# Optimization experiments

Measured on AMD Instinct MI355X. Metric: run time of the kernel, lower is better.

## Reference

```python
import jax, jax.numpy as jnp
import numpy as np

N = 10000      # nodes
E = 160000     # edges
F = 128        # feature multiplicity (num_features)
NSPEC = 10     # species
NL = 2         # interaction layers
R_MAX = 5.0
NB = 8         # bessel basis size
HR = 64        # radial MLP hidden
EPS = 0.5      # epsilon scaling
SH_DIM = 16    # l=0..3 -> 1+3+5+7
L_OF_LM = np.array([0, 1, 1, 1, 2, 2, 2, 2, 2, 3, 3, 3, 3, 3, 3, 3])
SLICES = [(0, 1), (1, 4), (4, 9), (9, 16)]  # (start,end) per l block


def _sh16(u):
    """Real spherical harmonics l=0..3, component normalization (sum_m Y^2 = 2l+1). u: [E,3] unit vectors."""
    x, y, z = u[:, 0], u[:, 1], u[:, 2]
    one = jnp.ones_like(x)
    s3, s5, s7, s15, s42, s70, s105 = map(lambda v: float(np.sqrt(v)), (3, 5, 7, 15, 42, 70, 105))
    ys = [
        one,
        s3 * x, s3 * y, s3 * z,
        s15 * x * y, s15 * y * z, 0.5 * s5 * (3 * z * z - 1.0), s15 * x * z, 0.5 * s15 * (x * x - y * y),
        0.25 * s70 * y * (3 * x * x - y * y),
        s105 * x * y * z,
        0.25 * s42 * y * (5 * z * z - 1.0),
        0.5 * s7 * (5 * z ** 3 - 3 * z),
        0.25 * s42 * x * (5 * z * z - 1.0),
        0.5 * s105 * z * (x * x - y * y),
        0.25 * s70 * x * (x * x - 3 * y * y),
    ]
    return jnp.stack(ys, axis=-1)  # [E,16]


def _radial(r):
    """Bessel radial basis with smooth cosine cutoff. r: [E,1] -> [E,NB]."""
    n = jnp.arange(1, NB + 1, dtype=r.dtype)
    f = jnp.sqrt(2.0 / R_MAX) * jnp.sin(n * jnp.pi * r / R_MAX) / jnp.maximum(r, 1e-9)
    cut = 0.5 * (jnp.cos(jnp.pi * jnp.clip(r, 0.0, R_MAX) / R_MAX) + 1.0)
    return f * cut


def setup_inputs() -> dict:
    key = jax.random.key(0)
    ks = jax.random.split(key, 16)
    d = {}
    d["vectors"] = jax.random.normal(ks[0], (E, 3), jnp.float32) * 1.5
    d["node_specie"] = jax.random.randint(ks[1], (N,), 0, NSPEC, jnp.int32)
    d["senders"] = jax.random.randint(ks[2], (E,), 0, N, jnp.int32)
    d["receivers"] = jax.random.randint(ks[3], (E,), 0, N, jnp.int32)
    d["emb_W"] = jax.random.normal(ks[4], (NSPEC, F), jnp.float32)
    d["radial_W1"] = jax.random.normal(ks[5], (NL, NB, HR), jnp.float32) / np.sqrt(NB)
    d["radial_b1"] = jnp.zeros((NL, HR), jnp.float32)
    d["radial_W2"] = jax.random.normal(ks[6], (NL, HR, F * 4), jnp.float32) / np.sqrt(HR)
    d["lin_W"] = jax.random.normal(ks[7], (NL, NSPEC, 4, F, F), jnp.float32) / np.sqrt(F)
    d["prod_c"] = jax.random.normal(ks[8], (NL, NSPEC, 3, F), jnp.float32) * 0.3
    d["sc_W"] = jax.random.normal(ks[9], (NL, NSPEC, 4, F, F), jnp.float32) / np.sqrt(F)
    d["ro0_W"] = jax.random.normal(ks[10], (F, 1), jnp.float32) / np.sqrt(F)
    d["ro1_W1"] = jax.random.normal(ks[11], (F, 16), jnp.float32) / np.sqrt(F)
    d["ro1_W2"] = jax.random.normal(ks[12], (16, 1), jnp.float32) / 4.0
    return d


def _species_linear(feats, W):
    # feats: [N,F,16], W: [N,4,F,F] (per-l linear). out[n,g,lm] = sum_f feats[n,f,lm] W[n,l(lm),f,g]
    outs = [jnp.einsum("nfm,nfg->ngm", feats[:, :, a:b], W[:, l]) for l, (a, b) in enumerate(SLICES)]
    return jnp.concatenate(outs, axis=-1)


def reference(vectors, node_specie, senders, receivers, emb_W, radial_W1, radial_b1,
              radial_W2, lin_W, prod_c, sc_W, ro0_W, ro1_W1, ro1_W2):
    lengths = jnp.maximum(jnp.linalg.norm(vectors, axis=-1, keepdims=True), 1e-9)  # [E,1]
    sh = _sh16(vectors / lengths)          # [E,16] edge attrs
    edge_feats = _radial(lengths)          # [E,NB]

    # node embedding: scalars only (l=0 slot)
    feats = jnp.zeros((N, F, SH_DIM), vectors.dtype).at[:, :, 0].set(emb_W[node_specie])
    lmap = jnp.asarray(L_OF_LM)
    outputs = []
    for i in range(NL):
        # radial MLP -> per-(feature,l) tensor-product weights
        h = jax.nn.silu(edge_feats @ radial_W1[i] + radial_b1[i])
        rw = (h @ radial_W2[i]).reshape(E, F, 4)          # [E,F,4]
        sender_scalars = feats[senders, :, 0]             # gather, [E,F]
        # per-edge tensor product: scalar x SH weighted by radial weights
        msg = sender_scalars[:, :, None] * rw[:, :, lmap] * sh[:, None, :]   # [E,F,16]
        agg = jax.ops.segment_sum(msg, receivers, num_segments=N)           # scatter-sum, [N,F,16]
        new = _species_linear(agg, lin_W[i][node_specie]) * EPS
        # residual self-connection (per-species linear) for layers > 0
        sc = None if i == 0 else _species_linear(feats, sc_W[i][node_specie])
        # product basis: correlation-3 polynomial in the scalar channel
        c = prod_c[i][node_specie]                         # [N,3,F]
        s = new[:, :, 0]
        poly = c[:, 0] + c[:, 1] * s + c[:, 2] * s * s     # [N,F]
        new = new * poly[:, :, None]
        feats = new if sc is None else new + sc
        scal = feats[:, :, 0]
        if i < NL - 1:
            outputs.append(scal @ ro0_W)                   # linear readout
        else:
            outputs.append(jax.nn.silu(scal @ ro1_W1) @ ro1_W2)  # nonlinear readout
    return jnp.stack(outputs, axis=1)  # [N, NL, 1]
```

## Files before the change

kernel.cpp:

```cpp
#include <hip/hip_runtime.h>
#include <math.h>
#include <stdint.h>

#define N_NODES 10000
#define N_EDGES 160000
#define F 128
#define NB 8
#define HR 64
#define NSPEC 10
#define PI_F 3.14159265358979323846f
#define NPAD 10160
#define NT_MAX 635
#define ETILES 2500

typedef unsigned short ushort_t;
typedef __attribute__((ext_vector_type(8))) short short8;
typedef __attribute__((ext_vector_type(4))) float f32x4;

__device__ __forceinline__ float silu_f(float x){ return x / (1.f + expf(-x)); }
__device__ __forceinline__ float bfu(ushort_t u) {
    union { unsigned int i; float f; } v; v.i = ((unsigned int)u) << 16; return v.f;
}
__device__ __forceinline__ ushort_t f2bf(float f) {
    union { float f; unsigned int i; } v; v.f = f;
    unsigned int x = v.i;
    unsigned int r = (x + 0x7fffu + ((x >> 16) & 1u)) >> 16;
    return (ushort_t)r;
}

__global__ __launch_bounds__(256) void k_conv_zero(
    const float* __restrict__ linW, const float* __restrict__ scW, const float* __restrict__ rW2,
    ushort_t* __restrict__ WBlin0, ushort_t* __restrict__ WBsc0, ushort_t* __restrict__ W2T0,
    int* __restrict__ zero_base)
{
    const int gtid = blockIdx.x*256 + threadIdx.x;
    const int GRID = 1984*256;
    for (int i = gtid; i < 2*N_NODES + 32; i += GRID) zero_base[i] = 0;
    const int LINTOT = 2*NSPEC*16384;
    const int SCTOT  = NSPEC*16384;
    int i = gtid;
    if (i < LINTOT) {
        int mat = i >> 14;
        int r = i & 16383;
        int fo = r >> 7, fi = r & 127;
        WBlin0[(size_t)mat*16384 + fo*128 + fi] =
            f2bf(linW[((size_t)mat*4 + 0)*16384 + fi*128 + fo]);
    } else if (i < LINTOT + SCTOT) {
        int t2 = i - LINTOT;
        int sp = t2 >> 14;
        int r = t2 & 16383;
        int fo = r >> 7, fi = r & 127;
        WBsc0[(size_t)sp*16384 + fo*128 + fi] =
            f2bf(scW[((size_t)(NSPEC + sp)*4 + 0)*16384 + fi*128 + fo]);
    } else if (i < LINTOT + SCTOT + 2*128*64) {
        int t2 = i - LINTOT - SCTOT;
        int l = t2 >> 13; int r = t2 & 8191; int f = r >> 6; int k = r & 63;
        W2T0[t2] = f2bf(rW2[(size_t)l*HR*512 + (size_t)k*512 + 4*f]);
    }
}

__global__ void k_hist(const int* __restrict__ spec, const int* __restrict__ recv,
                       int* __restrict__ scnt, int* __restrict__ counts)
{
    int i = blockIdx.x*256 + threadIdx.x;
    if (i < N_EDGES) atomicAdd(&counts[recv[i]], 1);
    if (i < N_NODES) atomicAdd(&scnt[spec[i]], 1);
}

__global__ __launch_bounds__(256) void k_sfill(
    const int* __restrict__ spec, const int* __restrict__ scnt,
    int* __restrict__ sptr, int* __restrict__ psptr,
    int* __restrict__ scur, int* __restrict__ perm,
    int* __restrict__ inv, int* __restrict__ specS, int* __restrict__ pn)
{
    __shared__ int sptrL[NSPEC+1], psptrL[NSPEC+1];
    const int t = threadIdx.x;
    if (t == 0) {
        int acc = 0, pacc = 0;
        for (int s = 0; s < NSPEC; ++s) {
            sptrL[s] = acc; psptrL[s] = pacc;
            acc += scnt[s];
            pacc += ((scnt[s] + 15) >> 4) << 4;
        }
        sptrL[NSPEC] = acc; psptrL[NSPEC] = pacc;
        if (blockIdx.x == 0) {
            for (int s = 0; s <= NSPEC; ++s) { sptr[s] = sptrL[s]; psptr[s] = psptrL[s]; }
        }
    }
    __syncthreads();
    int n = blockIdx.x*256 + t;
    if (n >= N_NODES) return;
    int s = spec[n];
    int pos = sptrL[s] + atomicAdd(&scur[s], 1);
    perm[pos] = n; inv[n] = pos; specS[pos] = s;
    pn[pos] = psptrL[s] + (pos - sptrL[s]);
}

__global__ __launch_bounds__(256) void k_scan_init(
    const int* __restrict__ counts, const int* __restrict__ perm, int* __restrict__ row_ptr,
    const int* __restrict__ specS, const int* __restrict__ pn,
    const float* __restrict__ embW, ushort_t* __restrict__ fB0)
{
    const int t = threadIdx.x;
    if (blockIdx.x == 0) {
        __shared__ int ps[256];
        int loc[40];
        int sum = 0;
        int base = t * 40;
        #pragma unroll
        for (int j = 0; j < 40; ++j) {
            int idx = base + j;
            int c = (idx < N_NODES) ? counts[perm[idx]] : 0;
            loc[j] = c; sum += c;
        }
        ps[t] = sum;
        __syncthreads();
        for (int off = 1; off < 256; off <<= 1) {
            int v = (t >= off) ? ps[t-off] : 0;
            __syncthreads();
            ps[t] += v;
            __syncthreads();
        }
        int ex = ps[t] - sum;
        #pragma unroll
        for (int j = 0; j < 40; ++j) {
            int idx = base + j;
            if (idx < N_NODES) row_ptr[idx] = ex;
            ex += loc[j];
        }
        if (t == 255) row_ptr[N_NODES] = ex;
    } else {
        int i = (blockIdx.x - 1)*256 + t;
        if (i < N_NODES*F) {
            int n = i >> 7, f = i & 127;
            fB0[(size_t)pn[n]*128 + f] = f2bf(embW[specS[n]*F + f]);
        }
    }
}

__global__ void k_fill_pre(const int* __restrict__ recv, const int* __restrict__ senders,
                           const int* __restrict__ inv, const int* __restrict__ pn,
                           const int* __restrict__ row_ptr, int* __restrict__ cursor,
                           const float* __restrict__ vec,
                           float* __restrict__ basis_pos, int* __restrict__ sndrow)
{
    int e = blockIdx.x*256 + threadIdx.x;
    if (e >= N_EDGES) return;
    int r = inv[recv[e]];
    int q = row_ptr[r] + atomicAdd(&cursor[r], 1);
    sndrow[q] = pn[inv[senders[e]]];
    float x = vec[e*3+0], y = vec[e*3+1], z = vec[e*3+2];
    float rr = sqrtf(x*x + y*y + z*z);
    rr = fmaxf(rr, 1e-9f);
    float rc = fminf(rr, 5.0f);
    float cut = 0.5f * (cosf(PI_F * rc * 0.2f) + 1.f);
    float pref = sqrtf(0.4f) * cut / rr;
    float B[8];
    #pragma unroll
    for (int k = 1; k <= 8; ++k) B[k-1] = pref * sinf(PI_F * 0.2f * (float)k * rr);
    float4* dst = (float4*)(basis_pos + (size_t)q*8);
    dst[0] = make_float4(B[0], B[1], B[2], B[3]);
    dst[1] = make_float4(B[4], B[5], B[6], B[7]);
}

__global__ __launch_bounds__(256) void k_rw(
    const float* __restrict__ basis_pos,
    const float* __restrict__ rW1,
    const float* __restrict__ rb1,
    const ushort_t* __restrict__ W2T0,
    ushort_t* __restrict__ rw0)
{
    __shared__ float W1s[2][NB*HR];
    __shared__ float b1s[2][HR];
    __shared__ ushort_t hB[4][16][72];
    __shared__ ushort_t rwS[4][2048];

    const int t = threadIdx.x;
    const int wv = t >> 6;
    const int lane = t & 63;
    const int j64 = lane;
    const int r16 = lane & 15;
    const int quad = lane >> 4;

    W1s[0][t] = rW1[t];       W1s[0][256 + t] = rW1[256 + t];
    W1s[1][t] = rW1[512 + t]; W1s[1][256 + t] = rW1[768 + t];
    if (t < HR) { b1s[0][t] = rb1[t]; b1s[1][t] = rb1[HR + t]; }

    const int p0 = blockIdx.x * 64 + wv * 16;
    __syncthreads();

    for (int l = 0; l < 2; ++l) {
        #pragma unroll 4
        for (int e = 0; e < 16; ++e) {
            const float4* B4 = (const float4*)(basis_pos + (size_t)(p0 + e)*8);
            float4 x0 = B4[0], x1 = B4[1];
            float a = b1s[l][j64];
            a = fmaf(x0.x, W1s[l][0*HR + j64], a);
            a = fmaf(x0.y, W1s[l][1*HR + j64], a);
            a = fmaf(x0.z, W1s[l][2*HR + j64], a);
            a = fmaf(x0.w, W1s[l][3*HR + j64], a);
            a = fmaf(x1.x, W1s[l][4*HR + j64], a);
            a = fmaf(x1.y, W1s[l][5*HR + j64], a);
            a = fmaf(x1.z, W1s[l][6*HR + j64], a);
            a = fmaf(x1.w, W1s[l][7*HR + j64], a);
            hB[wv][e][j64] = f2bf(a / (1.f + expf(-a)));
        }
        {
            short8 a0 = *(const short8*)&hB[wv][r16][quad*8];
            short8 a1 = *(const short8*)&hB[wv][r16][32 + quad*8];
            const ushort_t* W2l = W2T0 + l*8192;
            #pragma unroll
            for (int nt = 0; nt < 8; ++nt) {
                const int col = nt*16 + r16;
                short8 b0 = *(const short8*)(W2l + (size_t)col*64 + quad*8);
                short8 b1 = *(const short8*)(W2l + (size_t)col*64 + 32 + quad*8);
                f32x4 c = (f32x4){0.f, 0.f, 0.f, 0.f};
                c = __builtin_amdgcn_mfma_f32_16x16x32_bf16(a0, b0, c, 0, 0, 0);
                c = __builtin_amdgcn_mfma_f32_16x16x32_bf16(a1, b1, c, 0, 0, 0);
                #pragma unroll
                for (int r = 0; r < 4; ++r)
                    rwS[wv][(quad*4 + r)*128 + col] = f2bf(c[r]);
            }
        }
        {
            ushort_t* dst = rw0 + (size_t)l*N_EDGES*128 + (size_t)p0*128;
            #pragma unroll
            for (int q = 0; q < 4; ++q)
                *(short8*)(dst + q*512 + lane*8) = *(const short8*)(&rwS[wv][q*512 + lane*8]);
        }
    }
}

__global__ __launch_bounds__(256) void k_agg0(
    const int* __restrict__ row_ptr,
    const int* __restrict__ sndrow,
    const int* __restrict__ pn,
    const ushort_t* __restrict__ rw0l,
    const ushort_t* __restrict__ fB_in,
    ushort_t* __restrict__ aggB0)
{
    const int t = threadIdx.x;
    const int n = blockIdx.x*2 + (t >> 7);
    const int f = t & 127;
    const int p0 = row_ptr[n], p1 = row_ptr[n+1];
    float acc = 0.f;
    #pragma unroll 4
    for (int p = p0; p < p1; ++p) {
        const float sf = bfu(fB_in[(size_t)sndrow[p]*128 + f]);
        const float rl = bfu(rw0l[(size_t)p*128 + f]);
        acc = fmaf(sf, rl, acc);
    }
    aggB0[(size_t)pn[n]*128 + f] = f2bf(acc);
}

__device__ __forceinline__ int tile_to_spec(const int* __restrict__ psptr, int tile)
{
    int spec = 0;
    const int row = tile*16;
    #pragma unroll
    for (int s = 1; s < NSPEC; ++s)
        if (row >= psptr[s]) spec = s;
    return spec;
}

__global__ __launch_bounds__(256) void k_gemm_epi0(
    const ushort_t* __restrict__ aggB0,
    const ushort_t* __restrict__ WBlin0,
    const int* __restrict__ scnt, const int* __restrict__ sptr,
    const int* __restrict__ psptr, const int* __restrict__ perm,
    const float* __restrict__ prodc, const float* __restrict__ ro0,
    ushort_t* __restrict__ fB1, float* __restrict__ out)
{
    __shared__ float redS[16][65];
    const int tile = blockIdx.x;
    const int spec = tile_to_spec(psptr, tile);
    const int t = threadIdx.x;
    const int lane = t & 63;
    const int wv = t >> 6;
    const int r16 = lane & 15;
    const int quad = lane >> 4;

    const ushort_t* Ap = aggB0 + (size_t)tile*16*128;
    const ushort_t* Wp = WBlin0 + (size_t)spec*16384;
    const float* pc = prodc + (size_t)spec*3*F;

    short8 a[4];
    #pragma unroll
    for (int c = 0; c < 4; ++c)
        a[c] = *(const short8*)(Ap + (size_t)r16*128 + c*32 + quad*8);

    float pr[4] = {0.f, 0.f, 0.f, 0.f};
    #pragma unroll
    for (int nt = 0; nt < 2; ++nt) {
        const int col = wv*32 + nt*16 + r16;
        f32x4 acc = (f32x4){0.f, 0.f, 0.f, 0.f};
        #pragma unroll
        for (int c = 0; c < 4; ++c) {
            short8 b = *(const short8*)(Wp + (size_t)col*128 + c*32 + quad*8);
            acc = __builtin_amdgcn_mfma_f32_16x16x32_bf16(a[c], b, acc, 0, 0, 0);
        }
        const float w0 = ro0[col];
        const float p0c = pc[col], p1c = pc[F+col], p2c = pc[2*F+col];
        #pragma unroll
        for (int r = 0; r < 4; ++r) {
            float s = acc[r] * 0.5f;
            float val = s * (p0c + p1c*s + p2c*s*s);
            fB1[((size_t)tile*16 + quad*4 + r)*128 + col] = f2bf(val);
            pr[r] = fmaf(val, w0, pr[r]);
        }
    }
    #pragma unroll
    for (int r = 0; r < 4; ++r) redS[quad*4 + r][wv*16 + r16] = pr[r];
    __syncthreads();
    if (t < 16) {
        int rel = tile*16 + t - psptr[spec];
        if (rel >= 0 && rel < scnt[spec]) {
            float s = 0.f;
            for (int j = 0; j < 64; ++j) s += redS[t][j];
            out[(size_t)perm[sptr[spec] + rel]*2 + 0] = s;
        }
    }
}

__global__ __launch_bounds__(256) void k_gemm_epi1(
    const ushort_t* __restrict__ aggB0,
    const ushort_t* __restrict__ fB1,
    const ushort_t* __restrict__ WBlin1, const ushort_t* __restrict__ WBsc0,
    const int* __restrict__ scnt, const int* __restrict__ sptr,
    const int* __restrict__ psptr, const int* __restrict__ perm,
    const float* __restrict__ prodc,
    const float* __restrict__ ro1W1, const float* __restrict__ ro1W2,
    float* __restrict__ out)
{
    __shared__ float sS[16][132];
    __shared__ float yS[16][17];
    const int tile = blockIdx.x;
    const int spec = tile_to_spec(psptr, tile);
    const int t = threadIdx.x;
    const int lane = t & 63;
    const int wv = t >> 6;
    const int r16 = lane & 15;
    const int quad = lane >> 4;

    const ushort_t* Ap = aggB0 + (size_t)tile*16*128;
    const ushort_t* Fp = fB1   + (size_t)tile*16*128;
    const ushort_t* Wl = WBlin1 + (size_t)spec*16384;
    const ushort_t* Ws = WBsc0  + (size_t)spec*16384;
    const float* pc = prodc + ((size_t)NSPEC + spec)*3*F;

    short8 a1[4], a2[4];
    #pragma unroll
    for (int c = 0; c < 4; ++c) {
        a1[c] = *(const short8*)(Ap + (size_t)r16*128 + c*32 + quad*8);
        a2[c] = *(const short8*)(Fp + (size_t)r16*128 + c*32 + quad*8);
    }
    #pragma unroll
    for (int nt = 0; nt < 2; ++nt) {
        const int col = wv*32 + nt*16 + r16;
        f32x4 accl = (f32x4){0.f, 0.f, 0.f, 0.f};
        f32x4 accs = (f32x4){0.f, 0.f, 0.f, 0.f};
        #pragma unroll
        for (int c = 0; c < 4; ++c) {
            short8 bl = *(const short8*)(Wl + (size_t)col*128 + c*32 + quad*8);
            short8 bs = *(const short8*)(Ws + (size_t)col*128 + c*32 + quad*8);
            accl = __builtin_amdgcn_mfma_f32_16x16x32_bf16(a1[c], bl, accl, 0, 0, 0);
            accs = __builtin_amdgcn_mfma_f32_16x16x32_bf16(a2[c], bs, accs, 0, 0, 0);
        }
        const float p0c = pc[col], p1c = pc[F+col], p2c = pc[2*F+col];
        #pragma unroll
        for (int r = 0; r < 4; ++r) {
            float s = accl[r] * 0.5f;
            sS[quad*4 + r][col] = s * (p0c + p1c*s + p2c*s*s) + accs[r];
        }
    }
    __syncthreads();
    {
        const int node = t >> 4, c = t & 15;
        float a = 0.f;
        #pragma unroll 8
        for (int g = 0; g < F; ++g) a = fmaf(sS[node][g], ro1W1[g*16 + c], a);
        a = silu_f(a);
        yS[node][c] = a * ro1W2[c];
    }
    __syncthreads();
    if (t < 16) {
        int rel = tile*16 + t - psptr[spec];
        if (rel >= 0 && rel < scnt[spec]) {
            float s = 0.f;
            #pragma unroll
            for (int j = 0; j < 16; ++j) s += yS[t][j];
            out[(size_t)perm[sptr[spec] + rel]*2 + 1] = s;
        }
    }
}

extern "C" void kernel_launch(void* const* d_in, const int* in_sizes, int n_in,
                              void* d_out, int out_size, void* d_ws, size_t ws_size,
                              hipStream_t stream)
{
    (void)in_sizes; (void)n_in; (void)out_size; (void)ws_size;
    const float* vectors   = (const float*)d_in[0];
    const int*   spec      = (const int*)d_in[1];
    const int*   senders   = (const int*)d_in[2];
    const int*   receivers = (const int*)d_in[3];
    const float* embW      = (const float*)d_in[4];
    const float* rW1       = (const float*)d_in[5];
    const float* rb1       = (const float*)d_in[6];
    const float* rW2       = (const float*)d_in[7];
    const float* linW      = (const float*)d_in[8];
    const float* prodc     = (const float*)d_in[9];
    const float* scW       = (const float*)d_in[10];
    const float* ro0       = (const float*)d_in[11];
    const float* ro1W1     = (const float*)d_in[12];
    const float* ro1W2     = (const float*)d_in[13];
    float* out = (float*)d_out;

    char* ws = (char*)d_ws;
    float*    basis_pos = (float*)ws;    ws += sizeof(float)*(size_t)N_EDGES*8;
    ushort_t* rw0       = (ushort_t*)ws; ws += sizeof(ushort_t)*(size_t)2*N_EDGES*128;
    ushort_t* fB0       = (ushort_t*)ws; ws += sizeof(ushort_t)*(size_t)NPAD*128;
    ushort_t* fB1       = (ushort_t*)ws; ws += sizeof(ushort_t)*(size_t)NPAD*128;
    ushort_t* aggB0     = (ushort_t*)ws; ws += sizeof(ushort_t)*(size_t)NPAD*128;
    ushort_t* WBlin0    = (ushort_t*)ws; ws += sizeof(ushort_t)*(size_t)2*NSPEC*16384;
    ushort_t* WBsc0     = (ushort_t*)ws; ws += sizeof(ushort_t)*(size_t)NSPEC*16384;
    ushort_t* W2T0      = (ushort_t*)ws; ws += sizeof(ushort_t)*(size_t)2*128*64;
    int* sndrow    = (int*)ws; ws += sizeof(int)*N_EDGES;
    int* row_ptr   = (int*)ws; ws += sizeof(int)*(N_NODES+1);
    int* counts    = (int*)ws; ws += sizeof(int)*N_NODES;
    int* cursor    = (int*)ws; ws += sizeof(int)*N_NODES;
    int* scnt      = (int*)ws; ws += sizeof(int)*16;
    int* scur      = (int*)ws; ws += sizeof(int)*16;
    int* sptr      = (int*)ws; ws += sizeof(int)*16;
    int* psptr     = (int*)ws; ws += sizeof(int)*16;
    int* perm      = (int*)ws; ws += sizeof(int)*N_NODES;
    int* inv       = (int*)ws; ws += sizeof(int)*N_NODES;
    int* specS     = (int*)ws; ws += sizeof(int)*N_NODES;
    int* pn        = (int*)ws; ws += sizeof(int)*N_NODES;

    const int EB = (N_EDGES + 255)/256;

    k_conv_zero<<<1984, 256, 0, stream>>>(linW, scW, rW2, WBlin0, WBsc0, W2T0, counts);
    k_hist<<<EB, 256, 0, stream>>>(spec, receivers, scnt, counts);
    k_sfill<<<(N_NODES + 255)/256, 256, 0, stream>>>(spec, scnt, sptr, psptr, scur,
                                                     perm, inv, specS, pn);
    k_scan_init<<<1 + (N_NODES*F + 255)/256, 256, 0, stream>>>(counts, perm, row_ptr,
                                                               specS, pn, embW, fB0);
    k_fill_pre<<<EB, 256, 0, stream>>>(receivers, senders, inv, pn, row_ptr, cursor,
                                       vectors, basis_pos, sndrow);
    k_rw<<<ETILES, 256, 0, stream>>>(basis_pos, rW1, rb1, W2T0, rw0);

    k_agg0<<<N_NODES/2, 256, 0, stream>>>(row_ptr, sndrow, pn, rw0, fB0, aggB0);
    k_gemm_epi0<<<NT_MAX, 256, 0, stream>>>(aggB0, WBlin0, scnt, sptr, psptr, perm,
                                            prodc, ro0, fB1, out);
    k_agg0<<<N_NODES/2, 256, 0, stream>>>(row_ptr, sndrow, pn, rw0 + (size_t)N_EDGES*128, fB1, aggB0);
    k_gemm_epi1<<<NT_MAX, 256, 0, stream>>>(aggB0, fB1, WBlin0 + (size_t)NSPEC*16384, WBsc0,
                                            scnt, sptr, psptr, perm, prodc, ro1W1, ro1W2, out);
}
```

Baseline: 314.2 us.

## Fuse radial MLP with edge aggregation via segmented fp32 atomics

The per-edge radial-weight computation is merged with the message aggregation, one launch per layer. Edge tiles are sorted by receiver and each tile does a segmented reduction in shared memory, then adds into an fp32 node buffer with atomics. The buffer is converted to bf16 inside the GEMM kernels and cleared there for reuse. This removes the large bf16 radial-weight array written to and read back from global memory and drops the separate aggregation kernels. In exchange it adds atomic traffic at tile boundaries, makes the summation order nondeterministic, and recomputes the layer-1 radial MLP inside the second launch.

```diff
diff --git a/kernel.cpp b/kernel.cpp
--- a/kernel.cpp
+++ b/kernel.cpp
@@ -27,15 +27,22 @@
     unsigned int r = (x + 0x7fffu + ((x >> 16) & 1u)) >> 16;
     return (ushort_t)r;
 }
+__device__ __forceinline__ short8 pack8(const float* p) {
+    short8 r;
+    #pragma unroll
+    for (int i = 0; i < 8; ++i) r[i] = (short)f2bf(p[i]);
+    return r;
+}
 
 __global__ __launch_bounds__(256) void k_conv_zero(
     const float* __restrict__ linW, const float* __restrict__ scW, const float* __restrict__ rW2,
     ushort_t* __restrict__ WBlin0, ushort_t* __restrict__ WBsc0, ushort_t* __restrict__ W2T0,
-    int* __restrict__ zero_base)
+    int* __restrict__ zero_base, float* __restrict__ aggF)
 {
     const int gtid = blockIdx.x*256 + threadIdx.x;
     const int GRID = 1984*256;
     for (int i = gtid; i < 2*N_NODES + 32; i += GRID) zero_base[i] = 0;
+    for (int i = gtid; i < NPAD*128; i += GRID) aggF[i] = 0.f;
     const int LINTOT = 2*NSPEC*16384;
     const int SCTOT  = NSPEC*16384;
     int i = gtid;
@@ -142,13 +149,15 @@
                            const int* __restrict__ inv, const int* __restrict__ pn,
                            const int* __restrict__ row_ptr, int* __restrict__ cursor,
                            const float* __restrict__ vec,
-                           float* __restrict__ basis_pos, int* __restrict__ sndrow)
+                           float* __restrict__ basis_pos, int* __restrict__ sndrow,
+                           int* __restrict__ rcvrow)
 {
     int e = blockIdx.x*256 + threadIdx.x;
     if (e >= N_EDGES) return;
     int r = inv[recv[e]];
     int q = row_ptr[r] + atomicAdd(&cursor[r], 1);
     sndrow[q] = pn[inv[senders[e]]];
+    rcvrow[q] = pn[r];
     float x = vec[e*3+0], y = vec[e*3+1], z = vec[e*3+2];
     float rr = sqrtf(x*x + y*y + z*z);
     rr = fmaxf(rr, 1e-9f);
@@ -163,17 +172,22 @@
     dst[1] = make_float4(B[4], B[5], B[6], B[7]);
 }
 
-__global__ __launch_bounds__(256) void k_rw(
+__global__ __launch_bounds__(256) void k_rwagg(
+    const int layer,
     const float* __restrict__ basis_pos,
     const float* __restrict__ rW1,
     const float* __restrict__ rb1,
     const ushort_t* __restrict__ W2T0,
-    ushort_t* __restrict__ rw0)
-{
-    __shared__ float W1s[2][NB*HR];
-    __shared__ float b1s[2][HR];
+    const int* __restrict__ sndrow,
+    const int* __restrict__ rcvrow,
+    const ushort_t* __restrict__ fB_in,
+    float* __restrict__ aggF)
+{
+    __shared__ float W1s[NB*HR];
+    __shared__ float b1s[HR];
     __shared__ ushort_t hB[4][16][72];
-    __shared__ ushort_t rwS[4][2048];
+    __shared__ ushort_t rwS[4][16][132];
+    __shared__ int sndS[64], rowS[64];
 
     const int t = threadIdx.x;
     const int wv = t >> 6;
@@ -181,76 +195,68 @@
     const int j64 = lane;
     const int r16 = lane & 15;
     const int quad = lane >> 4;
-
-    W1s[0][t] = rW1[t];       W1s[0][256 + t] = rW1[256 + t];
-    W1s[1][t] = rW1[512 + t]; W1s[1][256 + t] = rW1[768 + t];
-    if (t < HR) { b1s[0][t] = rb1[t]; b1s[1][t] = rb1[HR + t]; }
-
-    const int p0 = blockIdx.x * 64 + wv * 16;
-    __syncthreads();
-
-    for (int l = 0; l < 2; ++l) {
-        #pragma unroll 4
-        for (int e = 0; e < 16; ++e) {
-            const float4* B4 = (const float4*)(basis_pos + (size_t)(p0 + e)*8);
-            float4 x0 = B4[0], x1 = B4[1];
-            float a = b1s[l][j64];
-            a = fmaf(x0.x, W1s[l][0*HR + j64], a);
-            a = fmaf(x0.y, W1s[l][1*HR + j64], a);
-            a = fmaf(x0.z, W1s[l][2*HR + j64], a);
-            a = fmaf(x0.w, W1s[l][3*HR + j64], a);
-            a = fmaf(x1.x, W1s[l][4*HR + j64], a);
-            a = fmaf(x1.y, W1s[l][5*HR + j64], a);
-            a = fmaf(x1.z, W1s[l][6*HR + j64], a);
-            a = fmaf(x1.w, W1s[l][7*HR + j64], a);
-            hB[wv][e][j64] = f2bf(a / (1.f + expf(-a)));
-        }
-        {
-            short8 a0 = *(const short8*)&hB[wv][r16][quad*8];
-            short8 a1 = *(const short8*)&hB[wv][r16][32 + quad*8];
-            const ushort_t* W2l = W2T0 + l*8192;
+    const int p0b = blockIdx.x * 64;
+
+    W1s[t] = rW1[layer*NB*HR + t];
+    W1s[256 + t] = rW1[layer*NB*HR + 256 + t];
+    if (t < HR) b1s[t] = rb1[layer*HR + t];
+    if (t < 64) { sndS[t] = sndrow[p0b + t]; rowS[t] = rcvrow[p0b + t]; }
+    __syncthreads();
+
+    const int p0 = p0b + wv*16;
+    #pragma unroll 4
+    for (int e = 0; e < 16; ++e) {
+        const float4* B4 = (const float4*)(basis_pos + (size_t)(p0 + e)*8);
+        float4 x0 = B4[0], x1 = B4[1];
+        float a = b1s[j64];
+        a = fmaf(x0.x, W1s[0*HR + j64], a);
+        a = fmaf(x0.y, W1s[1*HR + j64], a);
+        a = fmaf(x0.z, W1s[2*HR + j64], a);
+        a = fmaf(x0.w, W1s[3*HR + j64], a);
+        a = fmaf(x1.x, W1s[4*HR + j64], a);
+        a = fmaf(x1.y, W1s[5*HR + j64], a);
+        a = fmaf(x1.z, W1s[6*HR + j64], a);
+        a = fmaf(x1.w, W1s[7*HR + j64], a);
+        hB[wv][e][j64] = f2bf(a / (1.f + expf(-a)));
+    }
+    {
+        short8 a0 = *(const short8*)&hB[wv][r16][quad*8];
+        short8 a1 = *(const short8*)&hB[wv][r16][32 + quad*8];
+        const ushort_t* W2l = W2T0 + layer*8192;
+        #pragma unroll
+        for (int nt = 0; nt < 8; ++nt) {
+            const int col = nt*16 + r16;
+            short8 b0 = *(const short8*)(W2l + (size_t)col*64 + quad*8);
+            short8 b1 = *(const short8*)(W2l + (size_t)col*64 + 32 + quad*8);
+            f32x4 c = (f32x4){0.f, 0.f, 0.f, 0.f};
+            c = __builtin_amdgcn_mfma_f32_16x16x32_bf16(a0, b0, c, 0, 0, 0);
+            c = __builtin_amdgcn_mfma_f32_16x16x32_bf16(a1, b1, c, 0, 0, 0);
             #pragma unroll
-            for (int nt = 0; nt < 8; ++nt) {
-                const int col = nt*16 + r16;
-                short8 b0 = *(const short8*)(W2l + (size_t)col*64 + quad*8);
-                short8 b1 = *(const short8*)(W2l + (size_t)col*64 + 32 + quad*8);
-                f32x4 c = (f32x4){0.f, 0.f, 0.f, 0.f};
-                c = __builtin_amdgcn_mfma_f32_16x16x32_bf16(a0, b0, c, 0, 0, 0);
-                c = __builtin_amdgcn_mfma_f32_16x16x32_bf16(a1, b1, c, 0, 0, 0);
-                #pragma unroll
-                for (int r = 0; r < 4; ++r)
-                    rwS[wv][(quad*4 + r)*128 + col] = f2bf(c[r]);
+            for (int r = 0; r < 4; ++r)
+                rwS[wv][quad*4 + r][col] = f2bf(c[r]);
+        }
+    }
+    __syncthreads();
+
+    {
+        const int f = t & 127, mh = t >> 7;
+        const int base = mh*32;
+        int cur = rowS[base];
+        float acc = 0.f;
+        #pragma unroll 8
+        for (int i = 0; i < 32; ++i) {
+            const int pl = base + i;
+            const int row = rowS[pl];
+            const float sf = bfu(fB_in[(size_t)sndS[pl]*128 + f]);
+            const float rl = bfu(rwS[pl >> 4][pl & 15][f]);
+            if (row != cur) {
+                atomicAdd(&aggF[(size_t)cur*128 + f], acc);
+                cur = row; acc = 0.f;
             }
-        }
-        {
-            ushort_t* dst = rw0 + (size_t)l*N_EDGES*128 + (size_t)p0*128;
-            #pragma unroll
-            for (int q = 0; q < 4; ++q)
-                *(short8*)(dst + q*512 + lane*8) = *(const short8*)(&rwS[wv][q*512 + lane*8]);
-        }
-    }
-}
-
-__global__ __launch_bounds__(256) void k_agg0(
-    const int* __restrict__ row_ptr,
-    const int* __restrict__ sndrow,
-    const int* __restrict__ pn,
-    const ushort_t* __restrict__ rw0l,
-    const ushort_t* __restrict__ fB_in,
-    ushort_t* __restrict__ aggB0)
-{
-    const int t = threadIdx.x;
-    const int n = blockIdx.x*2 + (t >> 7);
-    const int f = t & 127;
-    const int p0 = row_ptr[n], p1 = row_ptr[n+1];
-    float acc = 0.f;
-    #pragma unroll 4
-    for (int p = p0; p < p1; ++p) {
-        const float sf = bfu(fB_in[(size_t)sndrow[p]*128 + f]);
-        const float rl = bfu(rw0l[(size_t)p*128 + f]);
-        acc = fmaf(sf, rl, acc);
-    }
-    aggB0[(size_t)pn[n]*128 + f] = f2bf(acc);
+            acc = fmaf(sf, rl, acc);
+        }
+        atomicAdd(&aggF[(size_t)cur*128 + f], acc);
+    }
 }
 
 __device__ __forceinline__ int tile_to_spec(const int* __restrict__ psptr, int tile)
@@ -264,7 +270,7 @@
 }
 
 __global__ __launch_bounds__(256) void k_gemm_epi0(
-    const ushort_t* __restrict__ aggB0,
+    float* __restrict__ aggF,
     const ushort_t* __restrict__ WBlin0,
     const int* __restrict__ scnt, const int* __restrict__ sptr,
     const int* __restrict__ psptr, const int* __restrict__ perm,
@@ -280,14 +286,20 @@
     const int r16 = lane & 15;
     const int quad = lane >> 4;
 
-    const ushort_t* Ap = aggB0 + (size_t)tile*16*128;
+    float* Ap = aggF + (size_t)tile*2048;
     const ushort_t* Wp = WBlin0 + (size_t)spec*16384;
     const float* pc = prodc + (size_t)spec*3*F;
 
     short8 a[4];
     #pragma unroll
     for (int c = 0; c < 4; ++c)
-        a[c] = *(const short8*)(Ap + (size_t)r16*128 + c*32 + quad*8);
+        a[c] = pack8(Ap + (size_t)r16*128 + c*32 + quad*8);
+    __syncthreads();
+    {
+        f32x4 z = (f32x4){0.f, 0.f, 0.f, 0.f};
+        *(f32x4*)(Ap + t*8) = z;
+        *(f32x4*)(Ap + t*8 + 4) = z;
+    }
 
     float pr[4] = {0.f, 0.f, 0.f, 0.f};
     #pragma unroll
@@ -323,7 +335,7 @@
 }
 
 __global__ __launch_bounds__(256) void k_gemm_epi1(
-    const ushort_t* __restrict__ aggB0,
+    const float* __restrict__ aggF,
     const ushort_t* __restrict__ fB1,
     const ushort_t* __restrict__ WBlin1, const ushort_t* __restrict__ WBsc0,
     const int* __restrict__ scnt, const int* __restrict__ sptr,
@@ -342,8 +354,8 @@
     const int r16 = lane & 15;
     const int quad = lane >> 4;
 
-    const ushort_t* Ap = aggB0 + (size_t)tile*16*128;
-    const ushort_t* Fp = fB1   + (size_t)tile*16*128;
+    const float* Ap = aggF + (size_t)tile*2048;
+    const ushort_t* Fp = fB1 + (size_t)tile*16*128;
     const ushort_t* Wl = WBlin1 + (size_t)spec*16384;
     const ushort_t* Ws = WBsc0  + (size_t)spec*16384;
     const float* pc = prodc + ((size_t)NSPEC + spec)*3*F;
@@ -351,7 +363,7 @@
     short8 a1[4], a2[4];
     #pragma unroll
     for (int c = 0; c < 4; ++c) {
-        a1[c] = *(const short8*)(Ap + (size_t)r16*128 + c*32 + quad*8);
+        a1[c] = pack8(Ap + (size_t)r16*128 + c*32 + quad*8);
         a2[c] = *(const short8*)(Fp + (size_t)r16*128 + c*32 + quad*8);
     }
     #pragma unroll
@@ -417,14 +429,14 @@
 
     char* ws = (char*)d_ws;
     float*    basis_pos = (float*)ws;    ws += sizeof(float)*(size_t)N_EDGES*8;
-    ushort_t* rw0       = (ushort_t*)ws; ws += sizeof(ushort_t)*(size_t)2*N_EDGES*128;
+    float*    aggF      = (float*)ws;    ws += sizeof(float)*(size_t)NPAD*128;
     ushort_t* fB0       = (ushort_t*)ws; ws += sizeof(ushort_t)*(size_t)NPAD*128;
     ushort_t* fB1       = (ushort_t*)ws; ws += sizeof(ushort_t)*(size_t)NPAD*128;
-    ushort_t* aggB0     = (ushort_t*)ws; ws += sizeof(ushort_t)*(size_t)NPAD*128;
     ushort_t* WBlin0    = (ushort_t*)ws; ws += sizeof(ushort_t)*(size_t)2*NSPEC*16384;
     ushort_t* WBsc0     = (ushort_t*)ws; ws += sizeof(ushort_t)*(size_t)NSPEC*16384;
     ushort_t* W2T0      = (ushort_t*)ws; ws += sizeof(ushort_t)*(size_t)2*128*64;
     int* sndrow    = (int*)ws; ws += sizeof(int)*N_EDGES;
+    int* rcvrow    = (int*)ws; ws += sizeof(int)*N_EDGES;
     int* row_ptr   = (int*)ws; ws += sizeof(int)*(N_NODES+1);
     int* counts    = (int*)ws; ws += sizeof(int)*N_NODES;
     int* cursor    = (int*)ws; ws += sizeof(int)*N_NODES;
@@ -439,20 +451,21 @@
 
     const int EB = (N_EDGES + 255)/256;
 
-    k_conv_zero<<<1984, 256, 0, stream>>>(linW, scW, rW2, WBlin0, WBsc0, W2T0, counts);
+    k_conv_zero<<<1984, 256, 0, stream>>>(linW, scW, rW2, WBlin0, WBsc0, W2T0, counts, aggF);
     k_hist<<<EB, 256, 0, stream>>>(spec, receivers, scnt, counts);
     k_sfill<<<(N_NODES + 255)/256, 256, 0, stream>>>(spec, scnt, sptr, psptr, scur,
                                                      perm, inv, specS, pn);
     k_scan_init<<<1 + (N_NODES*F + 255)/256, 256, 0, stream>>>(counts, perm, row_ptr,
                                                                specS, pn, embW, fB0);
     k_fill_pre<<<EB, 256, 0, stream>>>(receivers, senders, inv, pn, row_ptr, cursor,
-                                       vectors, basis_pos, sndrow);
-    k_rw<<<ETILES, 256, 0, stream>>>(basis_pos, rW1, rb1, W2T0, rw0);
-
-    k_agg0<<<N_NODES/2, 256, 0, stream>>>(row_ptr, sndrow, pn, rw0, fB0, aggB0);
-    k_gemm_epi0<<<NT_MAX, 256, 0, stream>>>(aggB0, WBlin0, scnt, sptr, psptr, perm,
+                                       vectors, basis_pos, sndrow, rcvrow);
+
+    k_rwagg<<<ETILES, 256, 0, stream>>>(0, basis_pos, rW1, rb1, W2T0,
+                                        sndrow, rcvrow, fB0, aggF);
+    k_gemm_epi0<<<NT_MAX, 256, 0, stream>>>(aggF, WBlin0, scnt, sptr, psptr, perm,
                                             prodc, ro0, fB1, out);
-    k_agg0<<<N_NODES/2, 256, 0, stream>>>(row_ptr, sndrow, pn, rw0 + (size_t)N_EDGES*128, fB1, aggB0);
-    k_gemm_epi1<<<NT_MAX, 256, 0, stream>>>(aggB0, fB1, WBlin0 + (size_t)NSPEC*16384, WBsc0,
+    k_rwagg<<<ETILES, 256, 0, stream>>>(1, basis_pos, rW1, rb1, W2T0,
+                                        sndrow, rcvrow, fB1, aggF);
+    k_gemm_epi1<<<NT_MAX, 256, 0, stream>>>(aggF, fB1, WBlin0 + (size_t)NSPEC*16384, WBsc0,
                                             scnt, sptr, psptr, perm, prodc, ro1W1, ro1W2, out);
 }
```

After: 317.3 us. Within noise of the previous version (+1.0%).
